# Kernel tuning notes

Measured on AMD Instinct MI355X. Metric: run time of the kernel, lower is better.

## Reference

```python
import jax, jax.numpy as jnp
import numpy as np

LN_EPS = 1e-5

def setup_inputs() -> dict:
    key = jax.random.key(0)
    ks = jax.random.split(key, 8)
    B, L, D, H = 4, 2048, 512, 8
    x = jax.random.normal(ks[0], (B, L, D), dtype=jnp.float32)
    token_ids = jax.random.randint(ks[1], (B, L), 0, 50000, dtype=jnp.int64)
    s = 1.0 / np.sqrt(D)
    Wq = jax.random.normal(ks[2], (D, D), dtype=jnp.float32) * s
    Wk = jax.random.normal(ks[3], (D, D), dtype=jnp.float32) * s
    Wv = jax.random.normal(ks[4], (D, D), dtype=jnp.float32) * s
    Wo = jax.random.normal(ks[5], (D, D), dtype=jnp.float32) * s
    gamma = jnp.ones((D,), dtype=jnp.float32)
    beta = jnp.zeros((D,), dtype=jnp.float32)
    return {"x": x, "token_ids": token_ids, "Wq": Wq, "Wk": Wk,
            "Wv": Wv, "Wo": Wo, "gamma": gamma, "beta": beta}

def reference(x, token_ids, Wq, Wk, Wv, Wo, gamma, beta):
    B, L, D = x.shape
    H = 8
    Dh = D // H
    residual = x
    # Pre-LN
    mu = jnp.mean(x, axis=-1, keepdims=True)
    var = jnp.mean(jnp.square(x - mu), axis=-1, keepdims=True)
    xn = (x - mu) * jax.lax.rsqrt(var + LN_EPS) * gamma + beta
    # projections (torch Linear: y = x @ W.T), split heads -> [B,H,L,Dh]
    def proj(W):
        return jnp.einsum('bld,ed->ble', xn, W).reshape(B, L, H, Dh).transpose(0, 2, 1, 3)
    Q, K, V = proj(Wq), proj(Wk), proj(Wv)
    scale = jnp.sqrt(jnp.float32(Dh))
    scores = jnp.einsum('bhqd,bhkd->bhqk', Q, K) / scale  # [B,H,L,L]
    neg_inf = jnp.float32(-jnp.inf)
    causal = jnp.triu(jnp.ones((L, L), dtype=bool), k=1)           # [L,L]
    pad = (token_ids == 0)[:, None, None, :]                       # [B,1,1,L]
    scores = jnp.where(causal[None, None], neg_inf, scores)
    scores = jnp.where(pad, neg_inf, scores)
    all_masked = jnp.all(jnp.isinf(scores), axis=-1, keepdims=True)
    scores = jnp.where(all_masked, 0.0, scores)
    attn = jax.nn.softmax(scores, axis=-1)  # dropout is identity in eval
    out = jnp.einsum('bhqk,bhkd->bhqd', attn, V)
    out = out.transpose(0, 2, 1, 3).reshape(B, L, D)
    out = jnp.einsum('bld,ed->ble', out, Wo)
    return residual + out
```

## Files before the change

kernel.cpp:

```cpp
#include <hip/hip_runtime.h>
#include <math.h>

typedef unsigned short u16;
typedef unsigned int u32;
typedef unsigned long long u64;
typedef float f32x4 __attribute__((ext_vector_type(4)));
typedef __bf16 bf16x8 __attribute__((ext_vector_type(8)));
typedef __bf16 bf16x4 __attribute__((ext_vector_type(4)));

constexpr int Bc = 4, Lc = 2048, Dc = 512, Hc = 8, DHc = 64;
constexpr int NTOK = Bc * Lc;
constexpr float LN_EPS = 1e-5f;
constexpr int KS = 72;
constexpr int PS = 72;
constexpr float QSCALE = 0.125f * 1.44269504088896340736f;

__device__ inline u16 bf_bits(float f) {
  return __builtin_bit_cast(u16, (__bf16)f);
}

__global__ __launch_bounds__(256) void prep_kernel(const float* __restrict__ s0,
                                                   const float* __restrict__ s1,
                                                   const float* __restrict__ s2,
                                                   const float* __restrict__ s3,
                                                   u16* __restrict__ d0,
                                                   u16* __restrict__ d1,
                                                   u16* __restrict__ d2,
                                                   u16* __restrict__ d3,
                                                   const int* __restrict__ tok,
                                                   u64* __restrict__ pm) {
  int bid = blockIdx.x;
  if (bid < 1024) {
    int mat = bid >> 8;
    int i = ((bid & 255) * 256 + threadIdx.x) * 4;
    const float* s = (mat == 0) ? s0 : (mat == 1) ? s1 : (mat == 2) ? s2 : s3;
    u16* d = (mat == 0) ? d0 : (mat == 1) ? d1 : (mat == 2) ? d2 : d3;
    float4 v = *(const float4*)&s[i];
    bf16x4 o;
    o[0] = (__bf16)v.x; o[1] = (__bf16)v.y; o[2] = (__bf16)v.z; o[3] = (__bf16)v.w;
    *(bf16x4*)&d[i] = o;
  } else {
    int wid = ((bid - 1024) * 256 + threadIdx.x) >> 6;
    int lane = threadIdx.x & 63;
    u64 m = __ballot(tok[(size_t)wid * 64 + lane] == 0);
    if (lane == 0) pm[wid] = m;
  }
}

__global__ __launch_bounds__(256) void ln_kernel(const float* __restrict__ x,
                                                 const float* __restrict__ gamma,
                                                 const float* __restrict__ beta,
                                                 u16* __restrict__ xn) {
  int wave = threadIdx.x >> 6;
  int lane = threadIdx.x & 63;
  int row  = blockIdx.x * 4 + wave;
  const float* xr = x + (size_t)row * Dc;
  float4 v0 = ((const float4*)xr)[lane * 2];
  float4 v1 = ((const float4*)xr)[lane * 2 + 1];
  float sum = v0.x + v0.y + v0.z + v0.w + v1.x + v1.y + v1.z + v1.w;
  float sq  = v0.x*v0.x + v0.y*v0.y + v0.z*v0.z + v0.w*v0.w
            + v1.x*v1.x + v1.y*v1.y + v1.z*v1.z + v1.w*v1.w;
  #pragma unroll
  for (int off = 32; off > 0; off >>= 1) {
    sum += __shfl_xor(sum, off);
    sq  += __shfl_xor(sq, off);
  }
  float mu = sum * (1.0f / Dc);
  float rs = rsqrtf(sq * (1.0f / Dc) - mu * mu + LN_EPS);
  float4 g0 = ((const float4*)gamma)[lane * 2];
  float4 g1 = ((const float4*)gamma)[lane * 2 + 1];
  float4 b0 = ((const float4*)beta)[lane * 2];
  float4 b1 = ((const float4*)beta)[lane * 2 + 1];
  bf16x8 o;
  o[0] = (__bf16)((v0.x - mu) * rs * g0.x + b0.x);
  o[1] = (__bf16)((v0.y - mu) * rs * g0.y + b0.y);
  o[2] = (__bf16)((v0.z - mu) * rs * g0.z + b0.z);
  o[3] = (__bf16)((v0.w - mu) * rs * g0.w + b0.w);
  o[4] = (__bf16)((v1.x - mu) * rs * g1.x + b1.x);
  o[5] = (__bf16)((v1.y - mu) * rs * g1.y + b1.y);
  o[6] = (__bf16)((v1.z - mu) * rs * g1.z + b1.z);
  o[7] = (__bf16)((v1.w - mu) * rs * g1.w + b1.w);
  *(bf16x8*)&xn[(size_t)row * Dc + lane * 8] = o;
}

template <int MODE>
__global__ __launch_bounds__(256) void gemm_bf16(const u16* __restrict__ A,
                                                 const u16* __restrict__ W,
                                                 const float* __restrict__ res,
                                                 float* __restrict__ out_f,
                                                 u16* __restrict__ o_q,
                                                 u16* __restrict__ o_k,
                                                 u16* __restrict__ o_v,
                                                 float* __restrict__ vm) {
  __shared__ u16 As[128 * KS];
  __shared__ u16 Bs[128 * KS];
  int tid = threadIdx.x;
  int lane = tid & 63;
  int w = tid >> 6;
  int wr = w >> 1, wc = w & 1;
  int cc = lane & 15, rb = lane >> 4;
  int n0 = blockIdx.x * 128;
  int e0 = blockIdx.y * 128;
  f32x4 acc[4][4] = {};
  for (int k0 = 0; k0 < Dc; k0 += 64) {
    #pragma unroll
    for (int u = 0; u < 4; u++) {
      int idx = u * 256 + tid;
      int row = idx >> 3;
      int col = (idx & 7) << 3;
      *(uint4*)&As[row * KS + col] = *(const uint4*)&A[(size_t)(n0 + row) * Dc + k0 + col];
      *(uint4*)&Bs[row * KS + col] = *(const uint4*)&W[(size_t)(e0 + row) * Dc + k0 + col];
    }
    __syncthreads();
    #pragma unroll
    for (int kk = 0; kk < 64; kk += 32) {
      bf16x8 aF[4], bF[4];
      #pragma unroll
      for (int m = 0; m < 4; m++)
        aF[m] = *(bf16x8*)&As[(wr * 64 + m * 16 + cc) * KS + kk + rb * 8];
      #pragma unroll
      for (int n = 0; n < 4; n++)
        bF[n] = *(bf16x8*)&Bs[(wc * 64 + n * 16 + cc) * KS + kk + rb * 8];
      #pragma unroll
      for (int m = 0; m < 4; m++)
        #pragma unroll
        for (int n = 0; n < 4; n++)
          acc[m][n] = __builtin_amdgcn_mfma_f32_16x16x32_bf16(aF[m], bF[n], acc[m][n], 0, 0, 0);
    }
    __syncthreads();
  }
  if (MODE == 3) {
    int bb = n0 >> 11;
    int mat = e0 >> 9;
    int e0c = e0 & 511;
    if (mat == 2) {
      #pragma unroll
      for (int n = 0; n < 4; n++) {
        int c = e0c + wc * 64 + n * 16 + cc;
        int h = c >> 6, dh = c & 63;
        float cp = 0.f;
        #pragma unroll
        for (int m = 0; m < 4; m++) {
          int l = (n0 + wr * 64 + m * 16 + rb * 4) & (Lc - 1);
          bf16x4 o4;
          o4[0] = (__bf16)acc[m][n][0]; o4[1] = (__bf16)acc[m][n][1];
          o4[2] = (__bf16)acc[m][n][2]; o4[3] = (__bf16)acc[m][n][3];
          size_t addr = ((((size_t)(bb * Hc + h)) * (Lc / 64) + (l >> 6)) * DHc + dh) * 64 + (l & 63);
          *(bf16x4*)&o_v[addr] = o4;
          cp += (acc[m][n][0] + acc[m][n][1]) + (acc[m][n][2] + acc[m][n][3]);
        }
        cp += __shfl_xor(cp, 16);
        cp += __shfl_xor(cp, 32);
        if (lane < 16) atomicAdd(&vm[(bb * Hc + h) * DHc + dh], cp);
      }
    } else {
      float sc = (mat == 0) ? QSCALE : 1.0f;
      u16* dst = (mat == 0) ? o_q : o_k;
      #pragma unroll
      for (int m = 0; m < 4; m++) {
        #pragma unroll
        for (int n = 0; n < 4; n++) {
          #pragma unroll
          for (int j = 0; j < 4; j++) {
            int r = n0 + wr * 64 + m * 16 + rb * 4 + j;
            int c = e0c + wc * 64 + n * 16 + cc;
            int ll = r & (Lc - 1);
            dst[(((size_t)(bb * Hc + (c >> 6))) * Lc + ll) * DHc + (c & 63)] = bf_bits(acc[m][n][j] * sc);
          }
        }
      }
    }
  } else {
    #pragma unroll
    for (int m = 0; m < 4; m++) {
      #pragma unroll
      for (int n = 0; n < 4; n++) {
        #pragma unroll
        for (int j = 0; j < 4; j++) {
          int r = n0 + wr * 64 + m * 16 + rb * 4 + j;
          int c = e0 + wc * 64 + n * 16 + cc;
          size_t o = (size_t)r * Dc + c;
          out_f[o] = acc[m][n][j] + res[o];
        }
      }
    }
  }
}

__global__ __launch_bounds__(256) void attn5(const u16* __restrict__ Q,
                                             const u16* __restrict__ K,
                                             const u16* __restrict__ VT,
                                             const float* __restrict__ vm,
                                             const u64* __restrict__ pmask,
                                             u16* __restrict__ out) {
  __shared__ u16 Ksh[2][4096];
  __shared__ u16 Vsh[2][4096];
  __shared__ u16 Ps[4][32 * PS];
  int tid = threadIdx.x;
  int w = tid >> 6;
  int lane = tid & 63;
  int cc = lane & 15, rb = lane >> 4;
  int bh = blockIdx.x;
  int qblk = (int)gridDim.y - 1 - (int)blockIdx.y;
  int q0 = qblk * 128 + w * 32;
  int b = bh >> 3, h = bh & 7;
  const u16* Qb = Q + (size_t)bh * Lc * DHc;
  const u16* Kb = K + (size_t)bh * Lc * DHc;
  const u16* Vb = VT + (size_t)bh * Lc * DHc;
  const u64* pmb = pmask + (b << 5);
  int own_last = q0 >> 6;
  int NT = 2 * qblk + 2;

  bf16x8 qF[2][2];
  #pragma unroll
  for (int qb = 0; qb < 2; qb++)
    #pragma unroll
    for (int kc = 0; kc < 2; kc++)
      qF[qb][kc] = *(const bf16x8*)&Qb[(size_t)(q0 + qb * 16 + cc) * DHc + kc * 32 + rb * 8];

  float mrow[2] = {-INFINITY, -INFINITY};
  float lrow[2] = {0.f, 0.f};
  f32x4 acc[2][4] = {};

  auto stage = [&](int kt, int buf) {
    const char* gK = (const char*)(Kb + (size_t)kt * 64 * DHc);
    const char* gV = (const char*)(Vb + (size_t)kt * 4096);
    #pragma unroll
    for (int i = 0; i < 2; i++) {
      int s = (i * 4 + w) * 64 + lane;
      int row = s >> 3;
      int src = row * 128 + (((s & 7) ^ (row & 7)) << 4);
      u16* lK = &Ksh[buf][(i * 4 + w) * 512];
      u16* lV = &Vsh[buf][(i * 4 + w) * 512];
      __builtin_amdgcn_global_load_lds(
          (const __attribute__((address_space(1))) void*)(gK + src),
          (__attribute__((address_space(3))) void*)lK, 16, 0, 0);
      __builtin_amdgcn_global_load_lds(
          (const __attribute__((address_space(1))) void*)(gV + src),
          (__attribute__((address_space(3))) void*)lV, 16, 0, 0);
    }
  };

  stage(0, 0);
  for (int kt = 0; kt < NT; kt++) {
    int cur = kt & 1;
    bool more = (kt + 1 < NT);
    if (more) stage(kt + 1, cur ^ 1);
    if (more) asm volatile("s_waitcnt vmcnt(4)" ::: "memory");
    else      asm volatile("s_waitcnt vmcnt(0)" ::: "memory");
    __builtin_amdgcn_sched_barrier(0);
    __builtin_amdgcn_s_barrier();
    __builtin_amdgcn_sched_barrier(0);

    if (kt <= own_last) {
      const u16* Kl = Ksh[cur];
      const u16* Vl = Vsh[cur];
      bool last = (kt == own_last);
      u64 pm = pmb[kt];
      int sw = cc & 7;
      f32x4 sq[2][4] = {};
      #pragma unroll
      for (int c = 0; c < 4; c++) {
        int krow = c * 16 + cc;
        bf16x8 kf0 = *(const bf16x8*)&Kl[krow * 64 + ((rb ^ sw) << 3)];
        bf16x8 kf1 = *(const bf16x8*)&Kl[krow * 64 + (((rb + 4) ^ sw) << 3)];
        __builtin_amdgcn_s_setprio(1);
        #pragma unroll
        for (int qb = 0; qb < 2; qb++) {
          sq[qb][c] = __builtin_amdgcn_mfma_f32_16x16x32_bf16(kf0, qF[qb][0], sq[qb][c], 0, 0, 0);
          sq[qb][c] = __builtin_amdgcn_mfma_f32_16x16x32_bf16(kf1, qF[qb][1], sq[qb][c], 0, 0, 0);
        }
        __builtin_amdgcn_s_setprio(0);
      }
      if (pm) {
        #pragma unroll
        for (int c = 0; c < 4; c++) {
          u32 smr = (((u32)(pm >> (c * 16)) & 0xffffu) >> (rb * 4));
          #pragma unroll
          for (int qb = 0; qb < 2; qb++)
            #pragma unroll
            for (int j = 0; j < 4; j++)
              if ((smr >> j) & 1) sq[qb][c][j] = -INFINITY;
        }
      }
      if (last) {
        #pragma unroll
        for (int qb = 0; qb < 2; qb++) {
          int qrel = q0 + qb * 16 + cc - kt * 64;
          #pragma unroll
          for (int c = 0; c < 4; c++)
            #pragma unroll
            for (int j = 0; j < 4; j++)
              if (c * 16 + rb * 4 + j > qrel) sq[qb][c][j] = -INFINITY;
        }
      }
      #pragma unroll
      for (int qb = 0; qb < 2; qb++) {
        float m0 = fmaxf(fmaxf(sq[qb][0][0], sq[qb][0][1]), fmaxf(sq[qb][0][2], sq[qb][0][3]));
        float m1 = fmaxf(fmaxf(sq[qb][1][0], sq[qb][1][1]), fmaxf(sq[qb][1][2], sq[qb][1][3]));
        float m2 = fmaxf(fmaxf(sq[qb][2][0], sq[qb][2][1]), fmaxf(sq[qb][2][2], sq[qb][2][3]));
        float m3 = fmaxf(fmaxf(sq[qb][3][0], sq[qb][3][1]), fmaxf(sq[qb][3][2], sq[qb][3][3]));
        float mx = fmaxf(fmaxf(m0, m1), fmaxf(m2, m3));
        mx = fmaxf(mx, __shfl_xor(mx, 16));
        mx = fmaxf(mx, __shfl_xor(mx, 32));
        if (!__all(mx <= mrow[qb] + 8.f)) {
          float nm = fmaxf(mrow[qb], mx);
          float nm2 = fmaxf(nm, -1e30f);
          float alpha = exp2f(mrow[qb] - nm2);
          lrow[qb] *= alpha;
          #pragma unroll
          for (int d0 = 0; d0 < 4; d0++)
            #pragma unroll
            for (int j = 0; j < 4; j++)
              acc[qb][d0][j] *= alpha;
          mrow[qb] = nm;
        }
        float nm2 = fmaxf(mrow[qb], -1e30f);
        float rs = 0.f;
        #pragma unroll
        for (int c = 0; c < 4; c++) {
          f32x4 p;
          #pragma unroll
          for (int j = 0; j < 4; j++) p[j] = exp2f(sq[qb][c][j] - nm2);
          rs += (p[0] + p[1]) + (p[2] + p[3]);
          bf16x4 p4;
          p4[0] = (__bf16)p[0]; p4[1] = (__bf16)p[1];
          p4[2] = (__bf16)p[2]; p4[3] = (__bf16)p[3];
          *(bf16x4*)&Ps[w][(qb * 16 + cc) * PS + c * 16 + rb * 4] = p4;
        }
        rs += __shfl_xor(rs, 16);
        rs += __shfl_xor(rs, 32);
        lrow[qb] += rs;
      }
      asm volatile("s_waitcnt lgkmcnt(0)" ::: "memory");
      __builtin_amdgcn_sched_barrier(0);
      __builtin_amdgcn_s_setprio(1);
      #pragma unroll
      for (int kc = 0; kc < 2; kc++) {
        bf16x8 pF0 = *(bf16x8*)&Ps[w][(size_t)cc * PS + kc * 32 + rb * 8];
        bf16x8 pF1 = *(bf16x8*)&Ps[w][(size_t)(16 + cc) * PS + kc * 32 + rb * 8];
        #pragma unroll
        for (int d0 = 0; d0 < 4; d0++) {
          int vrow = d0 * 16 + cc;
          bf16x8 vfv = *(const bf16x8*)&Vl[vrow * 64 + (((kc * 4 + rb) ^ sw) << 3)];
          acc[0][d0] = __builtin_amdgcn_mfma_f32_16x16x32_bf16(vfv, pF0, acc[0][d0], 0, 0, 0);
          acc[1][d0] = __builtin_amdgcn_mfma_f32_16x16x32_bf16(vfv, pF1, acc[1][d0], 0, 0, 0);
        }
      }
      __builtin_amdgcn_s_setprio(0);
    }
    __syncthreads();
  }

  #pragma unroll
  for (int qb = 0; qb < 2; qb++) {
    int q = q0 + qb * 16 + cc;
    bool ok = lrow[qb] > 0.f;
    float inv = ok ? 1.0f / lrow[qb] : 0.f;
    #pragma unroll
    for (int d0 = 0; d0 < 4; d0++) {
      bf16x4 o4;
      #pragma unroll
      for (int j = 0; j < 4; j++) {
        float v = ok ? acc[qb][d0][j] * inv
                     : vm[bh * DHc + d0 * 16 + rb * 4 + j] * (1.0f / Lc);
        o4[j] = (__bf16)v;
      }
      *(bf16x4*)&out[((size_t)(b * Lc + q)) * Dc + h * DHc + d0 * 16 + rb * 4] = o4;
    }
  }
}

extern "C" void kernel_launch(void* const* d_in, const int* in_sizes, int n_in,
                              void* d_out, int out_size, void* d_ws, size_t ws_size,
                              hipStream_t stream) {
  const float* x     = (const float*)d_in[0];
  const int*   tok   = (const int*)d_in[1];
  const float* Wq    = (const float*)d_in[2];
  const float* Wk    = (const float*)d_in[3];
  const float* Wv    = (const float*)d_in[4];
  const float* Wo    = (const float*)d_in[5];
  const float* gamma = (const float*)d_in[6];
  const float* beta  = (const float*)d_in[7];
  float* out = (float*)d_out;

  const size_t SEG = (size_t)NTOK * Dc;
  const size_t WSEG = (size_t)Dc * Dc;
  u16* xn   = (u16*)d_ws;
  u16* Qd   = xn + SEG;
  u16* Kd   = Qd + SEG;
  u16* VT   = Kd + SEG;
  u16* ao   = VT + SEG;
  u16* Wqkv = ao + SEG;
  u16* Wob  = Wqkv + 3 * WSEG;
  float* vm = (float*)(Wob + WSEG);
  u64* pmarr = (u64*)(vm + (size_t)Bc * Hc * DHc);

  (void)hipMemsetAsync(vm, 0, (size_t)Bc * Hc * DHc * sizeof(float), stream);

  prep_kernel<<<1056, 256, 0, stream>>>(Wq, Wk, Wv, Wo,
                                        Wqkv, Wqkv + WSEG, Wqkv + 2 * WSEG, Wob,
                                        tok, pmarr);
  ln_kernel<<<NTOK / 4, 256, 0, stream>>>(x, gamma, beta, xn);

  dim3 gq(NTOK / 128, (3 * Dc) / 128);
  gemm_bf16<3><<<gq, 256, 0, stream>>>(xn, Wqkv, nullptr, nullptr, Qd, Kd, VT, vm);

  dim3 ga(Bc * Hc, Lc / 128);
  attn5<<<ga, 256, 0, stream>>>(Qd, Kd, VT, vm, pmarr, ao);

  dim3 gg(NTOK / 128, Dc / 128);
  gemm_bf16<0><<<gg, 256, 0, stream>>>(ao, Wob, x, out, nullptr, nullptr, nullptr, nullptr);
}
```

Before: 127.4 us.

## Rewrite attention as single-wave blocks loading K/V directly from global memory

Replaces the 4-wave, 128-query attention block with one wave per 16-query tile. K and V fragments are read straight from global memory into registers, and the LDS double-buffering and block barriers are gone. Each iteration now covers 128 keys, and the row-sum reduction across lanes is deferred to the end. This removes LDS staging and synchronisation and gives finer causal load balance. In exchange, each block loses K/V reuse across waves, so global and L2 traffic grows and load latency is no longer hidden by a prefetch pipeline.

Measured after the change: 182.0 us. 1.43x slower.

```diff
diff --git a/kernel.cpp b/kernel.cpp
--- a/kernel.cpp
+++ b/kernel.cpp
@@ -12,8 +12,9 @@
 constexpr int NTOK = Bc * Lc;
 constexpr float LN_EPS = 1e-5f;
 constexpr int KS = 72;
-constexpr int PS = 72;
+constexpr int PS2 = 136;
 constexpr float QSCALE = 0.125f * 1.44269504088896340736f;
+constexpr float MNEG = -1e30f;
 
 __device__ inline u16 bf_bits(float f) {
   return __builtin_bit_cast(u16, (__bf16)f);
@@ -187,182 +188,159 @@
   }
 }
 
-__global__ __launch_bounds__(256) void attn5(const u16* __restrict__ Q,
+__global__ __launch_bounds__(64) void attn10(const u16* __restrict__ Q,
                                              const u16* __restrict__ K,
                                              const u16* __restrict__ VT,
                                              const float* __restrict__ vm,
                                              const u64* __restrict__ pmask,
                                              u16* __restrict__ out) {
-  __shared__ u16 Ksh[2][4096];
-  __shared__ u16 Vsh[2][4096];
-  __shared__ u16 Ps[4][32 * PS];
-  int tid = threadIdx.x;
-  int w = tid >> 6;
-  int lane = tid & 63;
+  __shared__ u16 Ps[16 * PS2];
+  int lane = threadIdx.x;
   int cc = lane & 15, rb = lane >> 4;
   int bh = blockIdx.x;
-  int qblk = (int)gridDim.y - 1 - (int)blockIdx.y;
-  int q0 = qblk * 128 + w * 32;
+  int qt = 127 - (int)blockIdx.y;
+  int q0 = qt * 16;
   int b = bh >> 3, h = bh & 7;
   const u16* Qb = Q + (size_t)bh * Lc * DHc;
   const u16* Kb = K + (size_t)bh * Lc * DHc;
   const u16* Vb = VT + (size_t)bh * Lc * DHc;
   const u64* pmb = pmask + (b << 5);
-  int own_last = q0 >> 6;
-  int NT = 2 * qblk + 2;
-
-  bf16x8 qF[2][2];
+  int nt = (q0 >> 7) + 1;
+
+  bf16x8 qF[2];
   #pragma unroll
-  for (int qb = 0; qb < 2; qb++)
+  for (int kc = 0; kc < 2; kc++)
+    qF[kc] = *(const bf16x8*)&Qb[(size_t)(q0 + cc) * DHc + kc * 32 + rb * 8];
+
+  float mrow = MNEG;
+  float lrow = 0.f;
+  f32x4 acc[4] = {};
+
+  for (int kt = 0; kt < nt; kt++) {
+    int k0 = kt << 7;
+    bool last = (kt == nt - 1);
+    u64 pm0 = pmb[kt * 2];
+    u64 pm1 = pmb[kt * 2 + 1];
+    f32x4 sq[8] = {};
+    #pragma unroll
+    for (int hf = 0; hf < 2; hf++) {
+      const u16* kp = Kb + (size_t)(k0 + hf * 64) * DHc;
+      bf16x8 kf[4][2];
+      #pragma unroll
+      for (int c = 0; c < 4; c++) {
+        kf[c][0] = *(const bf16x8*)&kp[(c * 16 + cc) * DHc + rb * 8];
+        kf[c][1] = *(const bf16x8*)&kp[(c * 16 + cc) * DHc + 32 + rb * 8];
+      }
+      __builtin_amdgcn_s_setprio(1);
+      #pragma unroll
+      for (int c = 0; c < 4; c++) {
+        sq[hf * 4 + c] = __builtin_amdgcn_mfma_f32_16x16x32_bf16(kf[c][0], qF[0], sq[hf * 4 + c], 0, 0, 0);
+        sq[hf * 4 + c] = __builtin_amdgcn_mfma_f32_16x16x32_bf16(kf[c][1], qF[1], sq[hf * 4 + c], 0, 0, 0);
+      }
+      __builtin_amdgcn_s_setprio(0);
+    }
+    __builtin_amdgcn_sched_barrier(0);
+    const u16* vp0 = Vb + (size_t)(kt * 2) * (DHc * 64);
+    bf16x8 vf[2][4];
     #pragma unroll
     for (int kc = 0; kc < 2; kc++)
-      qF[qb][kc] = *(const bf16x8*)&Qb[(size_t)(q0 + qb * 16 + cc) * DHc + kc * 32 + rb * 8];
-
-  float mrow[2] = {-INFINITY, -INFINITY};
-  float lrow[2] = {0.f, 0.f};
-  f32x4 acc[2][4] = {};
-
-  auto stage = [&](int kt, int buf) {
-    const char* gK = (const char*)(Kb + (size_t)kt * 64 * DHc);
-    const char* gV = (const char*)(Vb + (size_t)kt * 4096);
-    #pragma unroll
-    for (int i = 0; i < 2; i++) {
-      int s = (i * 4 + w) * 64 + lane;
-      int row = s >> 3;
-      int src = row * 128 + (((s & 7) ^ (row & 7)) << 4);
-      u16* lK = &Ksh[buf][(i * 4 + w) * 512];
-      u16* lV = &Vsh[buf][(i * 4 + w) * 512];
-      __builtin_amdgcn_global_load_lds(
-          (const __attribute__((address_space(1))) void*)(gK + src),
-          (__attribute__((address_space(3))) void*)lK, 16, 0, 0);
-      __builtin_amdgcn_global_load_lds(
-          (const __attribute__((address_space(1))) void*)(gV + src),
-          (__attribute__((address_space(3))) void*)lV, 16, 0, 0);
-    }
-  };
-
-  stage(0, 0);
-  for (int kt = 0; kt < NT; kt++) {
-    int cur = kt & 1;
-    bool more = (kt + 1 < NT);
-    if (more) stage(kt + 1, cur ^ 1);
-    if (more) asm volatile("s_waitcnt vmcnt(4)" ::: "memory");
-    else      asm volatile("s_waitcnt vmcnt(0)" ::: "memory");
+      #pragma unroll
+      for (int d0 = 0; d0 < 4; d0++)
+        vf[kc][d0] = *(const bf16x8*)&vp0[(d0 * 16 + cc) * 64 + kc * 32 + rb * 8];
+
+    if (pm0 | pm1) {
+      #pragma unroll
+      for (int c = 0; c < 8; c++) {
+        u64 pmw = (c < 4) ? pm0 : pm1;
+        u32 smr = (((u32)(pmw >> ((c & 3) * 16)) & 0xffffu) >> (rb * 4));
+        #pragma unroll
+        for (int j = 0; j < 4; j++)
+          if ((smr >> j) & 1) sq[c][j] = -INFINITY;
+      }
+    }
+    if (last) {
+      int qrel = (q0 & 127) + cc;
+      #pragma unroll
+      for (int c = 0; c < 8; c++)
+        #pragma unroll
+        for (int j = 0; j < 4; j++)
+          if (c * 16 + rb * 4 + j > qrel) sq[c][j] = -INFINITY;
+    }
+    {
+      float mh[8];
+      #pragma unroll
+      for (int c = 0; c < 8; c++)
+        mh[c] = fmaxf(fmaxf(sq[c][0], sq[c][1]), fmaxf(sq[c][2], sq[c][3]));
+      float mx = fmaxf(fmaxf(fmaxf(mh[0], mh[1]), fmaxf(mh[2], mh[3])),
+                       fmaxf(fmaxf(mh[4], mh[5]), fmaxf(mh[6], mh[7])));
+      if (!__all(mx <= mrow + 8.f)) {
+        float mf = fmaxf(mx, __shfl_xor(mx, 16));
+        mf = fmaxf(mf, __shfl_xor(mf, 32));
+        float nm = fmaxf(mrow, mf);
+        float alpha = exp2f(mrow - nm);
+        lrow *= alpha;
+        #pragma unroll
+        for (int d0 = 0; d0 < 4; d0++)
+          #pragma unroll
+          for (int j = 0; j < 4; j++)
+            acc[d0][j] *= alpha;
+        mrow = nm;
+      }
+      float rs = 0.f;
+      #pragma unroll
+      for (int c = 0; c < 8; c++) {
+        f32x4 p;
+        #pragma unroll
+        for (int j = 0; j < 4; j++) p[j] = exp2f(sq[c][j] - mrow);
+        rs += (p[0] + p[1]) + (p[2] + p[3]);
+        bf16x4 p4;
+        p4[0] = (__bf16)p[0]; p4[1] = (__bf16)p[1];
+        p4[2] = (__bf16)p[2]; p4[3] = (__bf16)p[3];
+        *(bf16x4*)&Ps[cc * PS2 + c * 16 + rb * 4] = p4;
+      }
+      lrow += rs;
+    }
+    asm volatile("s_waitcnt lgkmcnt(0)" ::: "memory");
     __builtin_amdgcn_sched_barrier(0);
-    __builtin_amdgcn_s_barrier();
-    __builtin_amdgcn_sched_barrier(0);
-
-    if (kt <= own_last) {
-      const u16* Kl = Ksh[cur];
-      const u16* Vl = Vsh[cur];
-      bool last = (kt == own_last);
-      u64 pm = pmb[kt];
-      int sw = cc & 7;
-      f32x4 sq[2][4] = {};
-      #pragma unroll
-      for (int c = 0; c < 4; c++) {
-        int krow = c * 16 + cc;
-        bf16x8 kf0 = *(const bf16x8*)&Kl[krow * 64 + ((rb ^ sw) << 3)];
-        bf16x8 kf1 = *(const bf16x8*)&Kl[krow * 64 + (((rb + 4) ^ sw) << 3)];
-        __builtin_amdgcn_s_setprio(1);
-        #pragma unroll
-        for (int qb = 0; qb < 2; qb++) {
-          sq[qb][c] = __builtin_amdgcn_mfma_f32_16x16x32_bf16(kf0, qF[qb][0], sq[qb][c], 0, 0, 0);
-          sq[qb][c] = __builtin_amdgcn_mfma_f32_16x16x32_bf16(kf1, qF[qb][1], sq[qb][c], 0, 0, 0);
-        }
-        __builtin_amdgcn_s_setprio(0);
-      }
-      if (pm) {
-        #pragma unroll
-        for (int c = 0; c < 4; c++) {
-          u32 smr = (((u32)(pm >> (c * 16)) & 0xffffu) >> (rb * 4));
-          #pragma unroll
-          for (int qb = 0; qb < 2; qb++)
-            #pragma unroll
-            for (int j = 0; j < 4; j++)
-              if ((smr >> j) & 1) sq[qb][c][j] = -INFINITY;
-        }
-      }
-      if (last) {
-        #pragma unroll
-        for (int qb = 0; qb < 2; qb++) {
-          int qrel = q0 + qb * 16 + cc - kt * 64;
-          #pragma unroll
-          for (int c = 0; c < 4; c++)
-            #pragma unroll
-            for (int j = 0; j < 4; j++)
-              if (c * 16 + rb * 4 + j > qrel) sq[qb][c][j] = -INFINITY;
-        }
-      }
-      #pragma unroll
-      for (int qb = 0; qb < 2; qb++) {
-        float m0 = fmaxf(fmaxf(sq[qb][0][0], sq[qb][0][1]), fmaxf(sq[qb][0][2], sq[qb][0][3]));
-        float m1 = fmaxf(fmaxf(sq[qb][1][0], sq[qb][1][1]), fmaxf(sq[qb][1][2], sq[qb][1][3]));
-        float m2 = fmaxf(fmaxf(sq[qb][2][0], sq[qb][2][1]), fmaxf(sq[qb][2][2], sq[qb][2][3]));
-        float m3 = fmaxf(fmaxf(sq[qb][3][0], sq[qb][3][1]), fmaxf(sq[qb][3][2], sq[qb][3][3]));
-        float mx = fmaxf(fmaxf(m0, m1), fmaxf(m2, m3));
-        mx = fmaxf(mx, __shfl_xor(mx, 16));
-        mx = fmaxf(mx, __shfl_xor(mx, 32));
-        if (!__all(mx <= mrow[qb] + 8.f)) {
-          float nm = fmaxf(mrow[qb], mx);
-          float nm2 = fmaxf(nm, -1e30f);
-          float alpha = exp2f(mrow[qb] - nm2);
-          lrow[qb] *= alpha;
-          #pragma unroll
-          for (int d0 = 0; d0 < 4; d0++)
-            #pragma unroll
-            for (int j = 0; j < 4; j++)
-              acc[qb][d0][j] *= alpha;
-          mrow[qb] = nm;
-        }
-        float nm2 = fmaxf(mrow[qb], -1e30f);
-        float rs = 0.f;
-        #pragma unroll
-        for (int c = 0; c < 4; c++) {
-          f32x4 p;
-          #pragma unroll
-          for (int j = 0; j < 4; j++) p[j] = exp2f(sq[qb][c][j] - nm2);
-          rs += (p[0] + p[1]) + (p[2] + p[3]);
-          bf16x4 p4;
-          p4[0] = (__bf16)p[0]; p4[1] = (__bf16)p[1];
-          p4[2] = (__bf16)p[2]; p4[3] = (__bf16)p[3];
-          *(bf16x4*)&Ps[w][(qb * 16 + cc) * PS + c * 16 + rb * 4] = p4;
-        }
-        rs += __shfl_xor(rs, 16);
-        rs += __shfl_xor(rs, 32);
-        lrow[qb] += rs;
-      }
-      asm volatile("s_waitcnt lgkmcnt(0)" ::: "memory");
-      __builtin_amdgcn_sched_barrier(0);
-      __builtin_amdgcn_s_setprio(1);
-      #pragma unroll
-      for (int kc = 0; kc < 2; kc++) {
-        bf16x8 pF0 = *(bf16x8*)&Ps[w][(size_t)cc * PS + kc * 32 + rb * 8];
-        bf16x8 pF1 = *(bf16x8*)&Ps[w][(size_t)(16 + cc) * PS + kc * 32 + rb * 8];
-        #pragma unroll
-        for (int d0 = 0; d0 < 4; d0++) {
-          int vrow = d0 * 16 + cc;
-          bf16x8 vfv = *(const bf16x8*)&Vl[vrow * 64 + (((kc * 4 + rb) ^ sw) << 3)];
-          acc[0][d0] = __builtin_amdgcn_mfma_f32_16x16x32_bf16(vfv, pF0, acc[0][d0], 0, 0, 0);
-          acc[1][d0] = __builtin_amdgcn_mfma_f32_16x16x32_bf16(vfv, pF1, acc[1][d0], 0, 0, 0);
-        }
-      }
-      __builtin_amdgcn_s_setprio(0);
-    }
-    __syncthreads();
-  }
-
-  #pragma unroll
-  for (int qb = 0; qb < 2; qb++) {
-    int q = q0 + qb * 16 + cc;
-    bool ok = lrow[qb] > 0.f;
-    float inv = ok ? 1.0f / lrow[qb] : 0.f;
+    __builtin_amdgcn_s_setprio(1);
+    #pragma unroll
+    for (int kc = 0; kc < 2; kc++) {
+      bf16x8 pF = *(bf16x8*)&Ps[(size_t)cc * PS2 + kc * 32 + rb * 8];
+      #pragma unroll
+      for (int d0 = 0; d0 < 4; d0++)
+        acc[d0] = __builtin_amdgcn_mfma_f32_16x16x32_bf16(vf[kc][d0], pF, acc[d0], 0, 0, 0);
+    }
+    __builtin_amdgcn_s_setprio(0);
+    const u16* vp1 = Vb + (size_t)(kt * 2 + 1) * (DHc * 64);
+    #pragma unroll
+    for (int kc = 0; kc < 2; kc++)
+      #pragma unroll
+      for (int d0 = 0; d0 < 4; d0++)
+        vf[kc][d0] = *(const bf16x8*)&vp1[(d0 * 16 + cc) * 64 + kc * 32 + rb * 8];
+    __builtin_amdgcn_s_setprio(1);
+    #pragma unroll
+    for (int kc = 0; kc < 2; kc++) {
+      bf16x8 pF = *(bf16x8*)&Ps[(size_t)cc * PS2 + 64 + kc * 32 + rb * 8];
+      #pragma unroll
+      for (int d0 = 0; d0 < 4; d0++)
+        acc[d0] = __builtin_amdgcn_mfma_f32_16x16x32_bf16(vf[kc][d0], pF, acc[d0], 0, 0, 0);
+    }
+    __builtin_amdgcn_s_setprio(0);
+  }
+
+  lrow += __shfl_xor(lrow, 16);
+  lrow += __shfl_xor(lrow, 32);
+
+  {
+    int q = q0 + cc;
+    bool ok = lrow > 0.f;
+    float inv = ok ? 1.0f / lrow : 0.f;
     #pragma unroll
     for (int d0 = 0; d0 < 4; d0++) {
       bf16x4 o4;
       #pragma unroll
       for (int j = 0; j < 4; j++) {
-        float v = ok ? acc[qb][d0][j] * inv
+        float v = ok ? acc[d0][j] * inv
                      : vm[bh * DHc + d0 * 16 + rb * 4 + j] * (1.0f / Lc);
         o4[j] = (__bf16)v;
       }
@@ -406,8 +384,8 @@
   dim3 gq(NTOK / 128, (3 * Dc) / 128);
   gemm_bf16<3><<<gq, 256, 0, stream>>>(xn, Wqkv, nullptr, nullptr, Qd, Kd, VT, vm);
 
-  dim3 ga(Bc * Hc, Lc / 128);
-  attn5<<<ga, 256, 0, stream>>>(Qd, Kd, VT, vm, pmarr, ao);
+  dim3 ga(Bc * Hc, 128);
+  attn10<<<ga, 64, 0, stream>>>(Qd, Kd, VT, vm, pmarr, ao);
 
   dim3 gg(NTOK / 128, Dc / 128);
   gemm_bf16<0><<<gg, 256, 0, stream>>>(ao, Wob, x, out, nullptr, nullptr, nullptr, nullptr);
```
